# Kernel tuning notes

Measured on AMD Instinct MI355X. Metric: run time of the kernel, lower is better.

Reference implementation:

```python
import jax, jax.numpy as jnp
import numpy as np


def _conv_same(x, w):
    # NHWC input, HWIO kernel, stride 1, SAME padding
    return jax.lax.conv_general_dilated(
        x, w, window_strides=(1, 1), padding='SAME',
        dimension_numbers=('NHWC', 'HWIO', 'NHWC'))


def _maxpool2(x):
    return jax.lax.reduce_window(
        x, -jnp.inf, jax.lax.max,
        window_dimensions=(1, 2, 2, 1), window_strides=(1, 2, 2, 1),
        padding='VALID')


def _binarize(x):
    # sign binarization with straight-through estimator (XNOR-net / Riptide)
    return x + jax.lax.stop_gradient(jnp.sign(x) - x)


def _binary_conv_relu(x, w):
    # BinaryConv2D: binarize activations and weights, conv, relu, no bias
    return jax.nn.relu(_conv_same(_binarize(x), _binarize(w)))


def setup_inputs() -> dict:
    key = jax.random.key(0)
    ks = jax.random.split(key, 32)
    d = {}
    d['x'] = jax.random.normal(ks[0], (128, 32, 32, 3), dtype=jnp.float32)
    d['w1'] = jax.random.normal(ks[1], (3, 3, 3, 128), dtype=jnp.float32) * 0.1
    d['b1'] = jax.random.normal(ks[2], (128,), dtype=jnp.float32) * 0.1
    chans = [128, 128, 256, 256, 512, 512]
    kshapes = [(3, 3, 128, 128), (3, 3, 128, 256), (3, 3, 256, 256),
               (3, 3, 256, 512), (3, 3, 512, 512)]
    for i, shp in zip(range(2, 7), kshapes):
        d[f'w{i}'] = jax.random.normal(ks[2 + i], shp, dtype=jnp.float32) * 0.1
    for i in range(1, 7):
        c = chans[i - 1]
        d[f'bn{i}_scale'] = jax.random.uniform(ks[10 + i], (c,), dtype=jnp.float32, minval=0.5, maxval=1.5)
        d[f'bn{i}_bias'] = jax.random.normal(ks[20 + i], (c,), dtype=jnp.float32) * 0.1
    d['dense_w'] = jax.random.normal(ks[30], (512, 10), dtype=jnp.float32) * 0.05
    d['dense_b'] = jax.random.normal(ks[31], (10,), dtype=jnp.float32) * 0.05
    return d


def reference(x, w1, b1, bn1_scale, bn1_bias, w2, bn2_scale, bn2_bias,
              w3, bn3_scale, bn3_bias, w4, bn4_scale, bn4_bias,
              w5, bn5_scale, bn5_bias, w6, bn6_scale, bn6_bias,
              dense_w, dense_b):
    # conv1: normal float conv + relu, then BN (inference: fused scale/bias)
    h = jax.nn.relu(_conv_same(x, w1) + b1)
    h = h * bn1_scale + bn1_bias
    # conv2 (binary) -> pool -> bn2
    h = _binary_conv_relu(h, w2)
    h = _maxpool2(h)
    h = h * bn2_scale + bn2_bias
    # conv3 (binary) -> bn3
    h = _binary_conv_relu(h, w3)
    h = h * bn3_scale + bn3_bias
    # conv4 (binary) -> pool -> bn4
    h = _binary_conv_relu(h, w4)
    h = _maxpool2(h)
    h = h * bn4_scale + bn4_bias
    # conv5 (binary) -> bn5
    h = _binary_conv_relu(h, w5)
    h = h * bn5_scale + bn5_bias
    # conv6 (binary) -> pool -> bn6
    h = _binary_conv_relu(h, w6)
    h = _maxpool2(h)  # -> [B, 4, 4, 512]
    h = h * bn6_scale + bn6_bias
    # Dense applied on last axis (original code has no flatten): [B,4,4,10]
    logits = jnp.einsum('bhwc,cd->bhwd', h, dense_w) + dense_b
    return jax.nn.softmax(logits, axis=-1)
```

## Files before the change

### kernel.cpp

```cpp
#include <hip/hip_runtime.h>
#include <cstdint>

typedef unsigned long long u64;

__global__ void zero_kernel(u64* __restrict__ p, int n) {
    int i = blockIdx.x * blockDim.x + threadIdx.x;
    int stride = gridDim.x * blockDim.x;
    for (; i < n; i += stride) p[i] = 0;
}

__global__ void pack_weights_kernel(const float* __restrict__ w, u64* __restrict__ wp,
                                    int Cin, int Cout) {
    int tid = blockIdx.x * blockDim.x + threadIdx.x;
    int wid = tid >> 6;
    int lane = threadIdx.x & 63;
    int Wi = Cin >> 6;
    int total = 9 * Wi * Cout;
    if (wid >= total) return;
    int oc = wid % Cout;
    int tw = wid / Cout;
    int tap = tw / Wi;
    int cw = tw % Wi;
    int ci = cw * 64 + lane;
    float v = w[((size_t)tap * Cin + ci) * Cout + oc];
    u64 mask = __ballot(v > 0.0f);
    if (lane == 0) wp[(size_t)tw * Cout + oc] = mask;
}

__global__ __launch_bounds__(128) void conv1_pack_kernel(
        const float* __restrict__ x, const float* __restrict__ w1,
        const float* __restrict__ b1, const float* __restrict__ s1,
        const float* __restrict__ bb1, u64* __restrict__ p1) {
    const int t = threadIdx.x;
    const int oc = t;
    const int bx = blockIdx.x;
    const int xseg = (bx & 3) << 3;
    const int y = (bx >> 2) & 31;
    const int b = bx >> 7;

    double wreg[27];
    #pragma unroll
    for (int k = 0; k < 27; k++) wreg[k] = (double)w1[k * 128 + oc];
    const double b1v = (double)b1[oc];
    const double tneg = -(double)bb1[oc] / (double)s1[oc];
    const bool always = tneg < 0.0;
    const double thr = tneg - b1v;

    double acc[8];
    #pragma unroll
    for (int i = 0; i < 8; i++) acc[i] = 0.0;

    #pragma unroll
    for (int ky = 0; ky < 3; ky++) {
        int iy = y - 1 + ky;
        if (iy < 0 || iy > 31) continue;
        #pragma unroll
        for (int col = 0; col < 10; col++) {
            int ix = xseg - 1 + col;
            if (ix < 0 || ix > 31) continue;
            const float* xp = x + ((b * 32 + iy) * 32 + ix) * 3;
            #pragma unroll
            for (int c = 0; c < 3; c++) {
                double xv = (double)xp[c];
                #pragma unroll
                for (int kx = 0; kx < 3; kx++) {
                    int px = col - kx;
                    if (px >= 0 && px < 8)
                        acc[px] += xv * wreg[(ky * 3 + kx) * 3 + c];
                }
            }
        }
    }
    #pragma unroll
    for (int px = 0; px < 8; px++) {
        bool bit = always || (acc[px] > thr);
        u64 m = __ballot(bit);
        if ((t & 63) == 0)
            p1[((size_t)(b * 34 + y + 1) * 34 + xseg + px + 1) * 2 + (t >> 6)] = m;
    }
}

template<int WI, int H, int W, int COUT, bool POOL, bool BITOUT>
__global__ __launch_bounds__(256) void bconv2_kernel(
        const u64* __restrict__ in, const u64* __restrict__ wp,
        const float* __restrict__ bns, const float* __restrict__ bnb,
        u64* __restrict__ outb, float* __restrict__ outf) {
    constexpr int ROWS = POOL ? 2 : 1;
    constexpr int NIR  = ROWS + 2;
    constexpr int Ho   = POOL ? H / 2 : H;
    constexpr int Wo   = POOL ? W / 2 : W;
    constexpr int WoW  = COUT >> 6;
    constexpr int Hp   = H + 2, Wp = W + 2;
    const int lane = threadIdx.x & 63;
    int wid = (blockIdx.x * blockDim.x + threadIdx.x) >> 6;
    wid = __builtin_amdgcn_readfirstlane(wid);
    const int wordo = wid % WoW;
    int t = wid / WoW;
    const int oy = t % Ho;
    const int b  = t / Ho;
    if (b >= 128) return;
    const int oc = wordo * 64 + lane;

    u64 wreg[9][WI];
    #pragma unroll
    for (int t9 = 0; t9 < 9; t9++)
        #pragma unroll
        for (int cw = 0; cw < WI; cw++)
            wreg[t9][cw] = wp[(size_t)(t9 * WI + cw) * COUT + oc];

    int pcwt[9];
    #pragma unroll
    for (int t9 = 0; t9 < 9; t9++) {
        int s = 0;
        #pragma unroll
        for (int cw = 0; cw < WI; cw++) s += (int)__popcll(wreg[t9][cw]);
        pcwt[t9] = s;
    }

    int m[ROWS][W];
    #pragma unroll
    for (int r = 0; r < ROWS; r++)
        #pragma unroll
        for (int c = 0; c < W; c++) m[r][c] = 0;

    const int base = POOL ? oy * 2 : oy;
    const u64* inb = in + ((size_t)b * Hp + base) * Wp * WI;

    #pragma unroll
    for (int ir = 0; ir < NIR; ir++) {
        const u64* inrow = inb + (size_t)ir * Wp * WI;
        #pragma unroll
        for (int c = 0; c < Wp; c++) {
            u64 av[WI];
            #pragma unroll
            for (int cw = 0; cw < WI; cw++) av[cw] = inrow[c * WI + cw];
            #pragma unroll
            for (int r = 0; r < ROWS; r++) {
                const int ky = ir - r;
                if (ky < 0 || ky > 2) continue;
                #pragma unroll
                for (int kx = 0; kx < 3; kx++) {
                    const int col = c - kx;
                    if (col < 0 || col >= W) continue;
                    int acc = 0;
                    #pragma unroll
                    for (int cw = 0; cw < WI; cw++)
                        acc += (int)__popcll(~(av[cw] ^ wreg[ky * 3 + kx][cw]));
                    m[r][col] += acc;
                }
            }
        }
    }

    const double sc = (double)bns[oc];
    const double bi = (double)bnb[oc];
    const double tf = -bi / sc;

    #pragma unroll
    for (int po = 0; po < Wo; po++) {
        int pmax = 0;
        #pragma unroll
        for (int r = 0; r < ROWS; r++) {
            #pragma unroll
            for (int wx = 0; wx < (POOL ? 2 : 1); wx++) {
                const int pc = POOL ? po * 2 + wx : po;
                const int pr = base + r;
                const bool top = (pr == 0), bot = (pr == H - 1);
                const bool lef = (pc == 0), rig = (pc == W - 1);
                int n_oob = 0, S = 0;
                if (top) { n_oob += 3; S += pcwt[0] + pcwt[1] + pcwt[2]; }
                if (bot) { n_oob += 3; S += pcwt[6] + pcwt[7] + pcwt[8]; }
                if (lef) { n_oob += 3; S += pcwt[0] + pcwt[3] + pcwt[6]; }
                if (rig) { n_oob += 3; S += pcwt[2] + pcwt[5] + pcwt[8]; }
                if (top && lef) { n_oob -= 1; S -= pcwt[0]; }
                if (top && rig) { n_oob -= 1; S -= pcwt[2]; }
                if (bot && lef) { n_oob -= 1; S -= pcwt[6]; }
                if (bot && rig) { n_oob -= 1; S -= pcwt[8]; }
                int d = 2 * m[r][pc] + 2 * S - 64 * WI * (9 + n_oob);
                pmax = d > pmax ? d : pmax;
            }
        }
        if constexpr (BITOUT) {
            u64 mask = __ballot((double)pmax > tf);
            if (lane == 0)
                outb[((size_t)(b * (Ho + 2) + oy + 1) * (Wo + 2) + po + 1) * WoW + wordo] = mask;
        } else {
            double h = (double)pmax * sc + bi;
            outf[((size_t)(b * Ho + oy) * Wo + po) * COUT + oc] = (float)h;
        }
    }
}

__global__ __launch_bounds__(256) void dense_softmax_kernel(
        const float* __restrict__ h6, const float* __restrict__ dw,
        const float* __restrict__ db, float* __restrict__ out) {
    int lane = threadIdx.x & 63;
    int r = (blockIdx.x * blockDim.x + threadIdx.x) >> 6;
    if (r >= 2048) return;
    const float* hr = h6 + (size_t)r * 512;
    float part[10];
    #pragma unroll
    for (int d = 0; d < 10; d++) part[d] = 0.f;
    #pragma unroll
    for (int k = 0; k < 8; k++) {
        int c = lane + 64 * k;
        float hv = hr[c];
        const float* dwr = dw + c * 10;
        #pragma unroll
        for (int d = 0; d < 10; d++) part[d] += hv * dwr[d];
    }
    #pragma unroll
    for (int off = 32; off >= 1; off >>= 1) {
        #pragma unroll
        for (int d = 0; d < 10; d++) part[d] += __shfl_down(part[d], off, 64);
    }
    if (lane == 0) {
        float logits[10];
        float mx = -1e30f;
        #pragma unroll
        for (int d = 0; d < 10; d++) { logits[d] = part[d] + db[d]; mx = fmaxf(mx, logits[d]); }
        float se = 0.f;
        #pragma unroll
        for (int d = 0; d < 10; d++) { logits[d] = expf(logits[d] - mx); se += logits[d]; }
        float inv = 1.f / se;
        #pragma unroll
        for (int d = 0; d < 10; d++) out[(size_t)r * 10 + d] = logits[d] * inv;
    }
}

extern "C" void kernel_launch(void* const* d_in, const int* in_sizes, int n_in,
                              void* d_out, int out_size, void* d_ws, size_t ws_size,
                              hipStream_t stream) {
    const float* x    = (const float*)d_in[0];
    const float* w1   = (const float*)d_in[1];
    const float* b1   = (const float*)d_in[2];
    const float* w2   = (const float*)d_in[3];
    const float* w3   = (const float*)d_in[4];
    const float* w4   = (const float*)d_in[5];
    const float* w5   = (const float*)d_in[6];
    const float* w6   = (const float*)d_in[7];
    const float* bn1s = (const float*)d_in[8];
    const float* bn1b = (const float*)d_in[9];
    const float* bn2s = (const float*)d_in[10];
    const float* bn2b = (const float*)d_in[11];
    const float* bn3s = (const float*)d_in[12];
    const float* bn3b = (const float*)d_in[13];
    const float* bn4s = (const float*)d_in[14];
    const float* bn4b = (const float*)d_in[15];
    const float* bn5s = (const float*)d_in[16];
    const float* bn5b = (const float*)d_in[17];
    const float* bn6s = (const float*)d_in[18];
    const float* bn6b = (const float*)d_in[19];
    const float* dw   = (const float*)d_in[20];
    const float* db   = (const float*)d_in[21];
    float* out = (float*)d_out;

    u64* ws  = (u64*)d_ws;
    u64* wp2 = ws;
    u64* wp3 = wp2 + 2304;
    u64* wp4 = wp3 + 4608;
    u64* wp5 = wp4 + 9216;
    u64* wp6 = wp5 + 18432;
    u64* p1  = wp6 + 36864;
    u64* p2  = p1 + 295936;
    u64* p3  = p2 + 82944;
    u64* p4  = p3 + 165888;
    u64* p5  = p4 + 51200;
    float* h6 = (float*)(p5 + 102400);
    const int NPAD = 295936 + 82944 + 165888 + 51200 + 102400;

    zero_kernel<<<1024, 256, 0, stream>>>(p1, NPAD);

    pack_weights_kernel<<<(9*2*128*64)/256, 256, 0, stream>>>(w2, wp2, 128, 128);
    pack_weights_kernel<<<(9*2*256*64)/256, 256, 0, stream>>>(w3, wp3, 128, 256);
    pack_weights_kernel<<<(9*4*256*64)/256, 256, 0, stream>>>(w4, wp4, 256, 256);
    pack_weights_kernel<<<(9*4*512*64)/256, 256, 0, stream>>>(w5, wp5, 256, 512);
    pack_weights_kernel<<<(9*8*512*64)/256, 256, 0, stream>>>(w6, wp6, 512, 512);

    conv1_pack_kernel<<<128*32*4, 128, 0, stream>>>(x, w1, b1, bn1s, bn1b, p1);

    bconv2_kernel<2,32,32,128,true, true ><<<1024, 256, 0, stream>>>(p1, wp2, bn2s, bn2b, p2, nullptr);
    bconv2_kernel<2,16,16,256,false,true ><<<2048, 256, 0, stream>>>(p2, wp3, bn3s, bn3b, p3, nullptr);
    bconv2_kernel<4,16,16,256,true, true ><<<1024, 256, 0, stream>>>(p3, wp4, bn4s, bn4b, p4, nullptr);
    bconv2_kernel<4,8,8,512,false,true ><<<2048, 256, 0, stream>>>(p4, wp5, bn5s, bn5b, p5, nullptr);
    bconv2_kernel<8,8,8,512,true, false><<<1024, 256, 0, stream>>>(p5, wp6, bn6s, bn6b, nullptr, h6);

    dense_softmax_kernel<<<2048*64/256, 256, 0, stream>>>(h6, dw, db, out);
}
```

Measured before the change: 376.8 us.

## Stream weights per kernel row, split output columns, and invert packed weight bits

The binary conv kernel stops holding all 9×WI weight words in registers. It now loops over kernel rows and channel chunks of at most four words, loading only the weights each chunk needs, and derives the border-correction sums incrementally. Output columns are split across XS wavefronts to add parallelism and shrink the accumulator arrays, and launch bounds request four blocks per SIMD-level occupancy. Weights are packed with inverted sign so the inner loop uses popcount(a^w) with no NOT. The costs are more global/L2 weight reloads and more halo input reads, and the non-unrolled loop adds some overhead.

```diff
diff --git a/kernel.cpp b/kernel.cpp
--- a/kernel.cpp
+++ b/kernel.cpp
@@ -23,7 +23,7 @@
     int cw = tw % Wi;
     int ci = cw * 64 + lane;
     float v = w[((size_t)tap * Cin + ci) * Cout + oc];
-    u64 mask = __ballot(v > 0.0f);
+    u64 mask = __ballot(!(v > 0.0f));
     if (lane == 0) wp[(size_t)tw * Cout + oc] = mask;
 }
 
@@ -80,73 +80,87 @@
     }
 }
 
-template<int WI, int H, int W, int COUT, bool POOL, bool BITOUT>
-__global__ __launch_bounds__(256) void bconv2_kernel(
+template<int WI, int H, int W, int COUT, bool POOL, int XS, bool BITOUT>
+__global__ __launch_bounds__(256, 4) void bconv3_kernel(
         const u64* __restrict__ in, const u64* __restrict__ wp,
         const float* __restrict__ bns, const float* __restrict__ bnb,
         u64* __restrict__ outb, float* __restrict__ outf) {
     constexpr int ROWS = POOL ? 2 : 1;
-    constexpr int NIR  = ROWS + 2;
     constexpr int Ho   = POOL ? H / 2 : H;
     constexpr int Wo   = POOL ? W / 2 : W;
     constexpr int WoW  = COUT >> 6;
     constexpr int Hp   = H + 2, Wp = W + 2;
+    constexpr int Wg   = W / XS;
+    constexpr int Wog  = Wo / XS;
+    constexpr int CH   = (WI < 4) ? WI : 4;
+    constexpr int NC   = WI / CH;
+
     const int lane = threadIdx.x & 63;
     int wid = (blockIdx.x * blockDim.x + threadIdx.x) >> 6;
     wid = __builtin_amdgcn_readfirstlane(wid);
     const int wordo = wid % WoW;
     int t = wid / WoW;
+    const int xg = t % XS; t /= XS;
     const int oy = t % Ho;
     const int b  = t / Ho;
     if (b >= 128) return;
     const int oc = wordo * 64 + lane;
-
-    u64 wreg[9][WI];
-    #pragma unroll
-    for (int t9 = 0; t9 < 9; t9++)
-        #pragma unroll
-        for (int cw = 0; cw < WI; cw++)
-            wreg[t9][cw] = wp[(size_t)(t9 * WI + cw) * COUT + oc];
-
-    int pcwt[9];
-    #pragma unroll
-    for (int t9 = 0; t9 < 9; t9++) {
-        int s = 0;
-        #pragma unroll
-        for (int cw = 0; cw < WI; cw++) s += (int)__popcll(wreg[t9][cw]);
-        pcwt[t9] = s;
-    }
-
-    int m[ROWS][W];
+    const int c0 = xg * Wg;
+    const int base = POOL ? oy * 2 : oy;
+
+    int m[ROWS][Wg];
     #pragma unroll
     for (int r = 0; r < ROWS; r++)
         #pragma unroll
-        for (int c = 0; c < W; c++) m[r][c] = 0;
-
-    const int base = POOL ? oy * 2 : oy;
-    const u64* inb = in + ((size_t)b * Hp + base) * Wp * WI;
-
-    #pragma unroll
-    for (int ir = 0; ir < NIR; ir++) {
-        const u64* inrow = inb + (size_t)ir * Wp * WI;
-        #pragma unroll
-        for (int c = 0; c < Wp; c++) {
-            u64 av[WI];
-            #pragma unroll
-            for (int cw = 0; cw < WI; cw++) av[cw] = inrow[c * WI + cw];
-            #pragma unroll
-            for (int r = 0; r < ROWS; r++) {
-                const int ky = ir - r;
-                if (ky < 0 || ky > 2) continue;
+        for (int c = 0; c < Wg; c++) m[r][c] = 0;
+
+    int S_top = 0, S_bot = 0, S_lef = 0, S_rig = 0;
+    int C_tl = 0, C_tr = 0, C_bl = 0, C_br = 0;
+
+    const u64* wbase = wp + oc;
+    const u64* inb = in + (((size_t)b * Hp + base) * Wp + c0) * WI;
+
+    #pragma unroll 1
+    for (int kc = 0; kc < 3 * NC; kc++) {
+        const int ky = kc / NC;
+        const int ch = kc % NC;
+        const int woff = ky * 3 * WI + ch * CH;
+        u64 wk[3][CH];
+        #pragma unroll
+        for (int kx = 0; kx < 3; kx++)
+            #pragma unroll
+            for (int cw = 0; cw < CH; cw++)
+                wk[kx][cw] = wbase[(size_t)(woff + kx * WI + cw) * COUT];
+
+        int pg[3];
+        #pragma unroll
+        for (int kx = 0; kx < 3; kx++) {
+            int s = 0;
+            #pragma unroll
+            for (int cw = 0; cw < CH; cw++) s += (int)__popcll(wk[kx][cw]);
+            pg[kx] = 64 * CH - s;
+        }
+        S_lef += pg[0]; S_rig += pg[2];
+        if (ky == 0) { S_top += pg[0] + pg[1] + pg[2]; C_tl += pg[0]; C_tr += pg[2]; }
+        if (ky == 2) { S_bot += pg[0] + pg[1] + pg[2]; C_bl += pg[0]; C_br += pg[2]; }
+
+        #pragma unroll
+        for (int r = 0; r < ROWS; r++) {
+            const u64* inrow = inb + (size_t)(r + ky) * Wp * WI + ch * CH;
+            #pragma unroll
+            for (int c = 0; c < Wg + 2; c++) {
+                u64 av[CH];
+                #pragma unroll
+                for (int cw = 0; cw < CH; cw++) av[cw] = inrow[(size_t)c * WI + cw];
                 #pragma unroll
                 for (int kx = 0; kx < 3; kx++) {
                     const int col = c - kx;
-                    if (col < 0 || col >= W) continue;
-                    int acc = 0;
+                    if (col < 0 || col >= Wg) continue;
+                    int acc = m[r][col];
                     #pragma unroll
-                    for (int cw = 0; cw < WI; cw++)
-                        acc += (int)__popcll(~(av[cw] ^ wreg[ky * 3 + kx][cw]));
-                    m[r][col] += acc;
+                    for (int cw = 0; cw < CH; cw++)
+                        acc += (int)__popcll(av[cw] ^ wk[kx][cw]);
+                    m[r][col] = acc;
                 }
             }
         }
@@ -154,39 +168,35 @@
 
     const double sc = (double)bns[oc];
     const double bi = (double)bnb[oc];
-    const double tf = -bi / sc;
-
-    #pragma unroll
-    for (int po = 0; po < Wo; po++) {
+
+    #pragma unroll
+    for (int po = 0; po < Wog; po++) {
         int pmax = 0;
         #pragma unroll
         for (int r = 0; r < ROWS; r++) {
             #pragma unroll
             for (int wx = 0; wx < (POOL ? 2 : 1); wx++) {
-                const int pc = POOL ? po * 2 + wx : po;
+                const int lc = POOL ? po * 2 + wx : po;
+                const int pc = c0 + lc;
                 const int pr = base + r;
-                const bool top = (pr == 0), bot = (pr == H - 1);
-                const bool lef = (pc == 0), rig = (pc == W - 1);
-                int n_oob = 0, S = 0;
-                if (top) { n_oob += 3; S += pcwt[0] + pcwt[1] + pcwt[2]; }
-                if (bot) { n_oob += 3; S += pcwt[6] + pcwt[7] + pcwt[8]; }
-                if (lef) { n_oob += 3; S += pcwt[0] + pcwt[3] + pcwt[6]; }
-                if (rig) { n_oob += 3; S += pcwt[2] + pcwt[5] + pcwt[8]; }
-                if (top && lef) { n_oob -= 1; S -= pcwt[0]; }
-                if (top && rig) { n_oob -= 1; S -= pcwt[2]; }
-                if (bot && lef) { n_oob -= 1; S -= pcwt[6]; }
-                if (bot && rig) { n_oob -= 1; S -= pcwt[8]; }
-                int d = 2 * m[r][pc] + 2 * S - 64 * WI * (9 + n_oob);
+                const int top = (pr == 0), bot = (pr == H - 1);
+                const int lef = (pc == 0), rig = (pc == W - 1);
+                int n_oob = 3 * (top + bot + lef + rig)
+                          - (top & lef) - (top & rig) - (bot & lef) - (bot & rig);
+                int S = top * S_top + bot * S_bot + lef * S_lef + rig * S_rig
+                      - (top & lef) * C_tl - (top & rig) * C_tr
+                      - (bot & lef) * C_bl - (bot & rig) * C_br;
+                int d = 2 * m[r][lc] + 2 * S - 64 * WI * (9 + n_oob);
                 pmax = d > pmax ? d : pmax;
             }
         }
+        double h = (double)pmax * sc + bi;
         if constexpr (BITOUT) {
-            u64 mask = __ballot((double)pmax > tf);
+            u64 mask = __ballot(h > 0.0);
             if (lane == 0)
-                outb[((size_t)(b * (Ho + 2) + oy + 1) * (Wo + 2) + po + 1) * WoW + wordo] = mask;
+                outb[((size_t)(b * (Ho + 2) + oy + 1) * (Wo + 2) + xg * Wog + po + 1) * WoW + wordo] = mask;
         } else {
-            double h = (double)pmax * sc + bi;
-            outf[((size_t)(b * Ho + oy) * Wo + po) * COUT + oc] = (float)h;
+            outf[((size_t)(b * Ho + oy) * Wo + xg * Wog + po) * COUT + oc] = (float)h;
         }
     }
 }
@@ -279,11 +289,11 @@
 
     conv1_pack_kernel<<<128*32*4, 128, 0, stream>>>(x, w1, b1, bn1s, bn1b, p1);
 
-    bconv2_kernel<2,32,32,128,true, true ><<<1024, 256, 0, stream>>>(p1, wp2, bn2s, bn2b, p2, nullptr);
-    bconv2_kernel<2,16,16,256,false,true ><<<2048, 256, 0, stream>>>(p2, wp3, bn3s, bn3b, p3, nullptr);
-    bconv2_kernel<4,16,16,256,true, true ><<<1024, 256, 0, stream>>>(p3, wp4, bn4s, bn4b, p4, nullptr);
-    bconv2_kernel<4,8,8,512,false,true ><<<2048, 256, 0, stream>>>(p4, wp5, bn5s, bn5b, p5, nullptr);
-    bconv2_kernel<8,8,8,512,true, false><<<1024, 256, 0, stream>>>(p5, wp6, bn6s, bn6b, nullptr, h6);
+    bconv3_kernel<2,32,32,128,true, 2,true ><<<2048, 256, 0, stream>>>(p1, wp2, bn2s, bn2b, p2, nullptr);
+    bconv3_kernel<2,16,16,256,false,1,true ><<<2048, 256, 0, stream>>>(p2, wp3, bn3s, bn3b, p3, nullptr);
+    bconv3_kernel<4,16,16,256,true, 2,true ><<<2048, 256, 0, stream>>>(p3, wp4, bn4s, bn4b, p4, nullptr);
+    bconv3_kernel<4,8,8,512,false,1,true ><<<2048, 256, 0, stream>>>(p4, wp5, bn5s, bn5b, p5, nullptr);
+    bconv3_kernel<8,8,8,512,true, 2,false><<<2048, 256, 0, stream>>>(p5, wp6, bn6s, bn6b, nullptr, h6);
 
     dense_softmax_kernel<<<2048*64/256, 256, 0, stream>>>(h6, dw, db, out);
 }
```

After: 359.4 us. 1.05x faster.
